# Performance work log

Hardware: AMD Instinct MI355X
Metric: run time of the kernel (lower is better)

The kernel has to match this reference:

```python
import jax, jax.numpy as jnp
import numpy as np

B, T, H, C = 64, 2048, 128, 7


def _lstm_layer(xs, W_ih, W_hh, b):
    # xs: [T, B, H_in]; PyTorch gate order i, f, g, o
    Bsz = xs.shape[1]
    Hs = W_hh.shape[1]

    def step(carry, x_t):
        h, c = carry
        gates = x_t @ W_ih.T + h @ W_hh.T + b  # [B, 4H]
        i, f, g, o = jnp.split(gates, 4, axis=-1)
        c = jax.nn.sigmoid(f) * c + jax.nn.sigmoid(i) * jnp.tanh(g)
        h = jax.nn.sigmoid(o) * jnp.tanh(c)
        return (h, c), h

    init = (jnp.zeros((Bsz, Hs), xs.dtype), jnp.zeros((Bsz, Hs), xs.dtype))
    _, ys = jax.lax.scan(step, init, xs)
    return ys  # [T, B, H]


def setup_inputs() -> dict:
    key = jax.random.key(0)
    ks = jax.random.split(key, 12)
    s = 1.0 / np.sqrt(H)
    u = lambda k, shape: jax.random.uniform(k, shape, jnp.float32, -s, s)
    x = jax.random.normal(ks[0], (B, T, 1), jnp.float32)
    lengths = jax.random.randint(ks[1], (B,), 1, T + 1, jnp.int32)
    return {
        "x": x,
        "lengths": lengths,
        "ff_w": u(ks[2], (H, 1)),
        "ff_b": u(ks[3], (H,)),
        "W_ih0": u(ks[4], (4 * H, H)),
        "W_hh0": u(ks[5], (4 * H, H)),
        "b0": u(ks[6], (4 * H,)),  # b_ih + b_hh fused
        "W_ih1": u(ks[7], (4 * H, H)),
        "W_hh1": u(ks[8], (4 * H, H)),
        "b1": u(ks[9], (4 * H,)),
        "lin_w": u(ks[10], (C, 3 * H)),
        "lin_b": u(ks[11], (C,)),
    }


def reference(x, lengths, ff_w, ff_b, W_ih0, W_hh0, b0, W_ih1, W_hh1, b1, lin_w, lin_b):
    # input projection (Linear(1, H))
    xf = x @ ff_w.T + ff_b  # [B, T, H]
    xs = jnp.transpose(xf, (1, 0, 2))  # [T, B, H]
    h1 = _lstm_layer(xs, W_ih0, W_hh0, b0)
    h2 = _lstm_layer(h1, W_ih1, W_hh1, b1)
    out = jnp.transpose(h2, (1, 0, 2))  # [B, T, H]

    # masked mean / max / last pooling over valid timesteps
    mask = jnp.arange(T)[None, :] < lengths[:, None]  # [B, T]
    mf = mask[:, :, None].astype(out.dtype)
    mean = (out * mf).sum(axis=1) / lengths[:, None].astype(out.dtype)
    mx = jnp.max(jnp.where(mask[:, :, None], out, -jnp.inf), axis=1)
    idx = jnp.broadcast_to((lengths - 1)[:, None, None], (out.shape[0], 1, out.shape[2]))
    last = jnp.take_along_axis(out, idx, axis=1)[:, 0]
    h = jnp.concatenate([mean, mx, last], axis=-1)  # [B, 3H]
    return h @ lin_w.T + lin_b  # [B, C]
```

## Files before the change

### kernel.cpp

```cpp
#include <hip/hip_runtime.h>
#include <hip/hip_fp16.h>

#define TT 2048
#define BB 64
#define HH 128
#define GG 512
#define CH 64
#define NCH (TT / CH)

typedef _Float16 f16x8 __attribute__((ext_vector_type(8)));
typedef _Float16 f16x4 __attribute__((ext_vector_type(4)));
typedef float f32x4 __attribute__((ext_vector_type(4)));

__device__ __forceinline__ float sigm(float x) {
    return __builtin_amdgcn_rcpf(1.0f + __expf(-x));
}
__device__ __forceinline__ float tanh_f(float x) {
    return 1.0f - 2.0f * __builtin_amdgcn_rcpf(1.0f + __expf(2.0f * x));
}
__device__ __forceinline__ void bar_lds() {
    asm volatile("s_waitcnt lgkmcnt(0)\n\ts_barrier" ::: "memory");
}

__device__ __forceinline__ f16x8 load_frag(const float* rowp, int kt, int lh) {
    const float4* p4 = (const float4*)(rowp + kt * 32 + lh * 8);
    float4 a = p4[0], b = p4[1];
    f16x8 f;
    f[0] = (_Float16)a.x; f[1] = (_Float16)a.y; f[2] = (_Float16)a.z; f[3] = (_Float16)a.w;
    f[4] = (_Float16)b.x; f[5] = (_Float16)b.y; f[6] = (_Float16)b.z; f[7] = (_Float16)b.w;
    return f;
}

__global__ __launch_bounds__(512, 1) void k_pipe(
    const float* __restrict__ x, const int* __restrict__ lengths,
    const float* __restrict__ ff_w, const float* __restrict__ ff_b,
    const float* __restrict__ W_ih0, const float* __restrict__ W_hh0,
    const float* __restrict__ b0, const float* __restrict__ W_ih1,
    const float* __restrict__ W_hh1, const float* __restrict__ b1,
    _Float16* __restrict__ h0g, int* __restrict__ flags,
    float* __restrict__ pooled) {
    const int tid = threadIdx.x;
    const int w = tid >> 6;
    const int lane = tid & 63;
    const int c = lane & 15;
    const int lh = lane >> 4;
    const int un = 16 * w + c;
    const bool ard = (c == 0);
    const bool wr16 = (lane < 16);

    __shared__ float xs[TT];
    __shared__ _Float16 Hb0[2][HH];
    __shared__ _Float16 Hb1[2][HH];
    __shared__ _Float16 Qs[CH][GG];

    if (blockIdx.x < BB) {
        const int b = blockIdx.x;
        for (int i = tid; i < TT; i += 512) xs[i] = x[b * TT + i];
        if (tid < 2 * HH) ((_Float16*)Hb0)[tid] = (_Float16)0.f;

        f16x8 Bf[4][4];
        float v[4], u0[4];
#pragma unroll
        for (int t2 = 0; t2 < 4; ++t2) {
            const int r = t2 * HH + un;
#pragma unroll
            for (int kt = 0; kt < 4; ++kt) Bf[t2][kt] = load_frag(W_hh0 + r * HH, kt, lh);
            const float4* wi4 = (const float4*)(W_ih0 + r * HH);
            const float4* fw4 = (const float4*)ff_w;
            const float4* fb4 = (const float4*)ff_b;
            float vv = 0.f, uu = 0.f;
#pragma unroll
            for (int m = 0; m < HH / 4; ++m) {
                float4 a = wi4[m], fw = fw4[m], fb = fb4[m];
                vv += a.x * fw.x + a.y * fw.y + a.z * fw.z + a.w * fw.w;
                uu += a.x * fb.x + a.y * fb.y + a.z * fb.z + a.w * fb.w;
            }
            v[t2] = vv;
            u0[t2] = uu + b0[r];
        }
#pragma unroll
        for (int t2 = 0; t2 < 4; ++t2)
#pragma unroll
            for (int kt = 0; kt < 4; ++kt) asm volatile("" : "+v"(Bf[t2][kt]));

        float cst0 = 0.f;
        f16x8 av[4];
#pragma unroll
        for (int kt = 0; kt < 4; ++kt) av[kt] = (f16x8){0, 0, 0, 0, 0, 0, 0, 0};
        __syncthreads();

#define PSTEP(T_, RB_)                                                          \
    do {                                                                        \
        if (ard) {                                                              \
            _Pragma("unroll") for (int kt = 0; kt < 4; ++kt)                    \
                av[kt] = *(const f16x8*)&Hb0[RB_][kt * 32 + lh * 8];            \
        }                                                                       \
        const float xt = xs[T_];                                                \
        float p[4];                                                             \
        _Pragma("unroll") for (int t2 = 0; t2 < 4; ++t2) {                      \
            f32x4 a;                                                            \
            a[0] = wr16 ? (xt * v[t2] + u0[t2]) : 0.f;                          \
            a[1] = 0.f; a[2] = 0.f; a[3] = 0.f;                                 \
            _Pragma("unroll") for (int kt = 0; kt < 4; ++kt)                    \
                a = __builtin_amdgcn_mfma_f32_16x16x32_f16(av[kt], Bf[t2][kt],  \
                                                           a, 0, 0, 0);         \
            p[t2] = a[0];                                                       \
        }                                                                       \
        float gi = sigm(p[0]), gf = sigm(p[1]);                                 \
        float gg = tanh_f(p[2]), go = sigm(p[3]);                               \
        cst0 = gf * cst0 + gi * gg;                                             \
        float h0n = go * tanh_f(cst0);                                          \
        if (wr16) {                                                             \
            Hb0[(RB_) ^ 1][un] = (_Float16)h0n;                                 \
            __builtin_nontemporal_store(                                        \
                (_Float16)h0n, h0g + ((size_t)b * TT + (T_)) * HH + un);        \
        }                                                                       \
        bar_lds();                                                              \
    } while (0)

        for (int ch = 0; ch < NCH; ++ch) {
            const int t0 = ch * CH;
            for (int j = 0; j < CH; j += 2) {
                PSTEP(t0 + j, 0);
                PSTEP(t0 + j + 1, 1);
            }
            __syncthreads();
            if (tid == 0)
                __hip_atomic_store(&flags[b * NCH + ch], ch + 1, __ATOMIC_RELEASE,
                                   __HIP_MEMORY_SCOPE_AGENT);
        }
#undef PSTEP
    } else {
        const int b = blockIdx.x - BB;
        if (tid < 2 * HH) ((_Float16*)Hb1)[tid] = (_Float16)0.f;

        f16x8 Bh[4][4];
        float bb1[4];
#pragma unroll
        for (int t2 = 0; t2 < 4; ++t2) {
#pragma unroll
            for (int kt = 0; kt < 4; ++kt)
                Bh[t2][kt] = load_frag(W_hh1 + (t2 * HH + un) * HH, kt, lh);
            bb1[t2] = b1[t2 * HH + un];
        }
#pragma unroll
        for (int t2 = 0; t2 < 4; ++t2)
#pragma unroll
            for (int kt = 0; kt < 4; ++kt) asm volatile("" : "+v"(Bh[t2][kt]));

        const int len = lengths[b];
        float cst1 = 0.f, mean = 0.f, mx = -1e30f, last = 0.f;
        f16x8 av[4];
#pragma unroll
        for (int kt = 0; kt < 4; ++kt) av[kt] = (f16x8){0, 0, 0, 0, 0, 0, 0, 0};
        __syncthreads();

#define CSTEP(T_, RB_)                                                          \
    do {                                                                        \
        const int jj = (T_) & (CH - 1);                                         \
        f16x4 qv = *(const f16x4*)&Qs[jj][un * 4];    \
        if (ard) {                                                              \
            _Pragma("unroll") for (int kt = 0; kt < 4; ++kt)                    \
                av[kt] = *(const f16x8*)&Hb1[RB_][kt * 32 + lh * 8];            \
        }                                                                       \
        float p[4];                                                             \
        _Pragma("unroll") for (int t2 = 0; t2 < 4; ++t2) {                      \
            f32x4 a;                                                            \
            a[0] = wr16 ? (float)qv[t2] : 0.f;                                  \
            a[1] = 0.f; a[2] = 0.f; a[3] = 0.f;                                 \
            _Pragma("unroll") for (int kt = 0; kt < 4; ++kt)                    \
                a = __builtin_amdgcn_mfma_f32_16x16x32_f16(av[kt], Bh[t2][kt],  \
                                                           a, 0, 0, 0);         \
            p[t2] = a[0];                                                       \
        }                                                                       \
        float gi = sigm(p[0]), gf = sigm(p[1]);                                 \
        float gg = tanh_f(p[2]), go = sigm(p[3]);                               \
        cst1 = gf * cst1 + gi * gg;                                             \
        float h1n = go * tanh_f(cst1);                                          \
        if (wr16) Hb1[(RB_) ^ 1][un] = (_Float16)h1n;                           \
        if ((T_) < len) {                                                       \
            mean += h1n;                                                        \
            mx = fmaxf(mx, h1n);                                                \
        }                                                                       \
        if ((T_) == len - 1) last = h1n;                                        \
        bar_lds();                                                              \
    } while (0)

        for (int ch = 0; ch < NCH; ++ch) {
            if (tid == 0) {
                int guard = 0;
                while (__hip_atomic_load(&flags[b * NCH + ch], __ATOMIC_ACQUIRE,
                                         __HIP_MEMORY_SCOPE_AGENT) != ch + 1) {
                    __builtin_amdgcn_s_sleep(8);
                    if (++guard > (1 << 22)) break;
                }
            }
            __syncthreads();
            f16x8 Bi[4][4];
#pragma unroll
            for (int t2 = 0; t2 < 4; ++t2)
#pragma unroll
                for (int kt = 0; kt < 4; ++kt)
                    Bi[t2][kt] = load_frag(W_ih1 + (t2 * HH + un) * HH, kt, lh);
            const _Float16* hbase = h0g + ((size_t)b * TT + ch * CH) * HH;
#pragma unroll
            for (int mt = 0; mt < 4; ++mt) {
                f16x8 am[4];
#pragma unroll
                for (int kt = 0; kt < 4; ++kt)
                    am[kt] = *(const f16x8*)(hbase + (mt * 16 + c) * HH + kt * 32 + lh * 8);
                f32x4 qa[4];
#pragma unroll
                for (int t2 = 0; t2 < 4; ++t2) {
                    qa[t2] = (f32x4){0.f, 0.f, 0.f, 0.f};
#pragma unroll
                    for (int kt = 0; kt < 4; ++kt)
                        qa[t2] = __builtin_amdgcn_mfma_f32_16x16x32_f16(
                            am[kt], Bi[t2][kt], qa[t2], 0, 0, 0);
                }
#pragma unroll
                for (int r = 0; r < 4; ++r) {
                    f16x4 qv;
#pragma unroll
                    for (int t2 = 0; t2 < 4; ++t2) qv[t2] = (_Float16)(qa[t2][r] + bb1[t2]);
                    *(f16x4*)&Qs[mt * 16 + 4 * lh + r][un * 4] = qv;
                }
            }
            __syncthreads();
            const int t0 = ch * CH;
            for (int j = 0; j < CH; j += 2) {
                CSTEP(t0 + j, 0);
                CSTEP(t0 + j + 1, 1);
            }
        }
#undef CSTEP
        if (wr16) {
            pooled[b * 384 + un] = mean / (float)len;
            pooled[b * 384 + 128 + un] = mx;
            pooled[b * 384 + 256 + un] = last;
        }
    }
}

__global__ __launch_bounds__(448) void k_head(
    const float* __restrict__ pooled, const float* __restrict__ lin_w,
    const float* __restrict__ lin_b, float* __restrict__ out) {
    int tid = threadIdx.x;
    int b = tid / 7, cc = tid % 7;
    const float* p = pooled + b * 384;
    const float* wr = lin_w + cc * 384;
    float a0 = 0.f, a1 = 0.f, a2 = 0.f, a3 = 0.f;
#pragma unroll
    for (int k = 0; k < 384; k += 4) {
        a0 += p[k + 0] * wr[k + 0];
        a1 += p[k + 1] * wr[k + 1];
        a2 += p[k + 2] * wr[k + 2];
        a3 += p[k + 3] * wr[k + 3];
    }
    out[tid] = lin_b[cc] + ((a0 + a1) + (a2 + a3));
}

extern "C" void kernel_launch(void* const* d_in, const int* in_sizes, int n_in,
                              void* d_out, int out_size, void* d_ws, size_t ws_size,
                              hipStream_t stream) {
    const float* x     = (const float*)d_in[0];
    const int*   lens  = (const int*)d_in[1];
    const float* ff_w  = (const float*)d_in[2];
    const float* ff_b  = (const float*)d_in[3];
    const float* W_ih0 = (const float*)d_in[4];
    const float* W_hh0 = (const float*)d_in[5];
    const float* b0    = (const float*)d_in[6];
    const float* W_ih1 = (const float*)d_in[7];
    const float* W_hh1 = (const float*)d_in[8];
    const float* b1    = (const float*)d_in[9];
    const float* lin_w = (const float*)d_in[10];
    const float* lin_b = (const float*)d_in[11];
    float* out = (float*)d_out;

    char* ws = (char*)d_ws;
    const size_t HBYTES = (size_t)BB * TT * HH * 2;
    _Float16* h0g = (_Float16*)ws;
    int* flags    = (int*)(ws + HBYTES);
    float* pooled = (float*)(ws + HBYTES + 8192);

    k_pipe<<<dim3(2 * BB), dim3(512), 0, stream>>>(
        x, lens, ff_w, ff_b, W_ih0, W_hh0, b0, W_ih1, W_hh1, b1, h0g, flags, pooled);
    k_head<<<dim3(1), dim3(448), 0, stream>>>(pooled, lin_w, lin_b, out);
}
```

Baseline: 1.384 ms.

## Process two batch elements per workgroup to interleave independent recurrences

Each workgroup now carries two independent batch sequences through the LSTM recurrence, halving the grid from 128 to 64 blocks. The two chains' MFMA and activation work are interleaved inside each timestep. This is meant to hide the latency of the serial per-step MFMA chain and share one barrier per step across two sequences. In exchange, each step carries twice the work, LDS use grows, and fewer CUs are occupied.

```diff
diff --git a/kernel.cpp b/kernel.cpp
--- a/kernel.cpp
+++ b/kernel.cpp
@@ -7,6 +7,7 @@
 #define GG 512
 #define CH 64
 #define NCH (TT / CH)
+#define NPB 32
 
 typedef _Float16 f16x8 __attribute__((ext_vector_type(8)));
 typedef _Float16 f16x4 __attribute__((ext_vector_type(4)));
@@ -48,15 +49,17 @@
     const bool ard = (c == 0);
     const bool wr16 = (lane < 16);
 
-    __shared__ float xs[TT];
-    __shared__ _Float16 Hb0[2][HH];
-    __shared__ _Float16 Hb1[2][HH];
-    __shared__ _Float16 Qs[CH][GG];
-
-    if (blockIdx.x < BB) {
-        const int b = blockIdx.x;
-        for (int i = tid; i < TT; i += 512) xs[i] = x[b * TT + i];
-        if (tid < 2 * HH) ((_Float16*)Hb0)[tid] = (_Float16)0.f;
+    __shared__ float xs[2][TT];
+    __shared__ _Float16 Hb0[2][2][HH];
+    __shared__ _Float16 Hb1[2][2][HH];
+    __shared__ _Float16 Qs[2][CH][GG];
+
+    if (blockIdx.x < NPB) {
+        const int p = blockIdx.x;
+        const int bA = p, bB = p + NPB;
+        for (int i = tid; i < 2 * TT; i += 512)
+            xs[i >> 11][i & (TT - 1)] = x[(i < TT ? bA : bB) * TT + (i & (TT - 1))];
+        if (tid < 4 * HH) ((_Float16*)Hb0)[tid] = (_Float16)0.f;
 
         f16x8 Bf[4][4];
         float v[4], u0[4];
@@ -83,37 +86,60 @@
 #pragma unroll
             for (int kt = 0; kt < 4; ++kt) asm volatile("" : "+v"(Bf[t2][kt]));
 
-        float cst0 = 0.f;
-        f16x8 av[4];
-#pragma unroll
-        for (int kt = 0; kt < 4; ++kt) av[kt] = (f16x8){0, 0, 0, 0, 0, 0, 0, 0};
+        float cstA = 0.f, cstB = 0.f;
+        f16x8 avA[4], avB[4];
+#pragma unroll
+        for (int kt = 0; kt < 4; ++kt) {
+            avA[kt] = (f16x8){0, 0, 0, 0, 0, 0, 0, 0};
+            avB[kt] = (f16x8){0, 0, 0, 0, 0, 0, 0, 0};
+        }
         __syncthreads();
 
 #define PSTEP(T_, RB_)                                                          \
     do {                                                                        \
         if (ard) {                                                              \
-            _Pragma("unroll") for (int kt = 0; kt < 4; ++kt)                    \
-                av[kt] = *(const f16x8*)&Hb0[RB_][kt * 32 + lh * 8];            \
-        }                                                                       \
-        const float xt = xs[T_];                                                \
-        float p[4];                                                             \
+            _Pragma("unroll") for (int kt = 0; kt < 4; ++kt) {                  \
+                avA[kt] = *(const f16x8*)&Hb0[0][RB_][kt * 32 + lh * 8];        \
+                avB[kt] = *(const f16x8*)&Hb0[1][RB_][kt * 32 + lh * 8];        \
+            }                                                                   \
+        }                                                                       \
+        const float xtA = xs[0][T_], xtB = xs[1][T_];                           \
+        float pA[4], pB[4];                                                     \
         _Pragma("unroll") for (int t2 = 0; t2 < 4; ++t2) {                      \
-            f32x4 a;                                                            \
-            a[0] = wr16 ? (xt * v[t2] + u0[t2]) : 0.f;                          \
-            a[1] = 0.f; a[2] = 0.f; a[3] = 0.f;                                 \
-            _Pragma("unroll") for (int kt = 0; kt < 4; ++kt)                    \
-                a = __builtin_amdgcn_mfma_f32_16x16x32_f16(av[kt], Bf[t2][kt],  \
-                                                           a, 0, 0, 0);         \
-            p[t2] = a[0];                                                       \
-        }                                                                       \
-        float gi = sigm(p[0]), gf = sigm(p[1]);                                 \
-        float gg = tanh_f(p[2]), go = sigm(p[3]);                               \
-        cst0 = gf * cst0 + gi * gg;                                             \
-        float h0n = go * tanh_f(cst0);                                          \
-        if (wr16) {                                                             \
-            Hb0[(RB_) ^ 1][un] = (_Float16)h0n;                                 \
-            __builtin_nontemporal_store(                                        \
-                (_Float16)h0n, h0g + ((size_t)b * TT + (T_)) * HH + un);        \
+            f32x4 aA, aB;                                                       \
+            aA[0] = wr16 ? (xtA * v[t2] + u0[t2]) : 0.f;                        \
+            aA[1] = 0.f; aA[2] = 0.f; aA[3] = 0.f;                              \
+            aB[0] = wr16 ? (xtB * v[t2] + u0[t2]) : 0.f;                        \
+            aB[1] = 0.f; aB[2] = 0.f; aB[3] = 0.f;                              \
+            _Pragma("unroll") for (int kt = 0; kt < 4; ++kt) {                  \
+                aA = __builtin_amdgcn_mfma_f32_16x16x32_f16(avA[kt],            \
+                         Bf[t2][kt], aA, 0, 0, 0);                              \
+                aB = __builtin_amdgcn_mfma_f32_16x16x32_f16(avB[kt],            \
+                         Bf[t2][kt], aB, 0, 0, 0);                              \
+            }                                                                   \
+            pA[t2] = aA[0]; pB[t2] = aB[0];                                     \
+        }                                                                       \
+        {                                                                       \
+            float gi = sigm(pA[0]), gf = sigm(pA[1]);                           \
+            float gg = tanh_f(pA[2]), go = sigm(pA[3]);                         \
+            cstA = gf * cstA + gi * gg;                                         \
+            float hn = go * tanh_f(cstA);                                       \
+            if (wr16) {                                                         \
+                Hb0[0][(RB_) ^ 1][un] = (_Float16)hn;                           \
+                __builtin_nontemporal_store(                                    \
+                    (_Float16)hn, h0g + ((size_t)bA * TT + (T_)) * HH + un);    \
+            }                                                                   \
+        }                                                                       \
+        {                                                                       \
+            float gi = sigm(pB[0]), gf = sigm(pB[1]);                           \
+            float gg = tanh_f(pB[2]), go = sigm(pB[3]);                         \
+            cstB = gf * cstB + gi * gg;                                         \
+            float hn = go * tanh_f(cstB);                                       \
+            if (wr16) {                                                         \
+                Hb0[1][(RB_) ^ 1][un] = (_Float16)hn;                           \
+                __builtin_nontemporal_store(                                    \
+                    (_Float16)hn, h0g + ((size_t)bB * TT + (T_)) * HH + un);    \
+            }                                                                   \
         }                                                                       \
         bar_lds();                                                              \
     } while (0)
@@ -126,13 +152,14 @@
             }
             __syncthreads();
             if (tid == 0)
-                __hip_atomic_store(&flags[b * NCH + ch], ch + 1, __ATOMIC_RELEASE,
+                __hip_atomic_store(&flags[p * NCH + ch], ch + 1, __ATOMIC_RELEASE,
                                    __HIP_MEMORY_SCOPE_AGENT);
         }
 #undef PSTEP
     } else {
-        const int b = blockIdx.x - BB;
-        if (tid < 2 * HH) ((_Float16*)Hb1)[tid] = (_Float16)0.f;
+        const int p = blockIdx.x - NPB;
+        const int bA = p, bB = p + NPB;
+        if (tid < 4 * HH) ((_Float16*)Hb1)[tid] = (_Float16)0.f;
 
         f16x8 Bh[4][4];
         float bb1[4];
@@ -148,48 +175,69 @@
 #pragma unroll
             for (int kt = 0; kt < 4; ++kt) asm volatile("" : "+v"(Bh[t2][kt]));
 
-        const int len = lengths[b];
-        float cst1 = 0.f, mean = 0.f, mx = -1e30f, last = 0.f;
-        f16x8 av[4];
-#pragma unroll
-        for (int kt = 0; kt < 4; ++kt) av[kt] = (f16x8){0, 0, 0, 0, 0, 0, 0, 0};
+        const int lenA = lengths[bA], lenB = lengths[bB];
+        float cstA = 0.f, cstB = 0.f;
+        float meanA = 0.f, meanB = 0.f, mxA = -1e30f, mxB = -1e30f;
+        float lastA = 0.f, lastB = 0.f;
+        f16x8 avA[4], avB[4];
+#pragma unroll
+        for (int kt = 0; kt < 4; ++kt) {
+            avA[kt] = (f16x8){0, 0, 0, 0, 0, 0, 0, 0};
+            avB[kt] = (f16x8){0, 0, 0, 0, 0, 0, 0, 0};
+        }
         __syncthreads();
 
 #define CSTEP(T_, RB_)                                                          \
     do {                                                                        \
         const int jj = (T_) & (CH - 1);                                         \
-        f16x4 qv = *(const f16x4*)&Qs[jj][un * 4];    \
+        f16x4 qA = *(const f16x4*)&Qs[0][jj][un * 4];                           \
+        f16x4 qB = *(const f16x4*)&Qs[1][jj][un * 4];                           \
         if (ard) {                                                              \
-            _Pragma("unroll") for (int kt = 0; kt < 4; ++kt)                    \
-                av[kt] = *(const f16x8*)&Hb1[RB_][kt * 32 + lh * 8];            \
-        }                                                                       \
-        float p[4];                                                             \
+            _Pragma("unroll") for (int kt = 0; kt < 4; ++kt) {                  \
+                avA[kt] = *(const f16x8*)&Hb1[0][RB_][kt * 32 + lh * 8];        \
+                avB[kt] = *(const f16x8*)&Hb1[1][RB_][kt * 32 + lh * 8];        \
+            }                                                                   \
+        }                                                                       \
+        float pA[4], pB[4];                                                     \
         _Pragma("unroll") for (int t2 = 0; t2 < 4; ++t2) {                      \
-            f32x4 a;                                                            \
-            a[0] = wr16 ? (float)qv[t2] : 0.f;                                  \
-            a[1] = 0.f; a[2] = 0.f; a[3] = 0.f;                                 \
-            _Pragma("unroll") for (int kt = 0; kt < 4; ++kt)                    \
-                a = __builtin_amdgcn_mfma_f32_16x16x32_f16(av[kt], Bh[t2][kt],  \
-                                                           a, 0, 0, 0);         \
-            p[t2] = a[0];                                                       \
-        }                                                                       \
-        float gi = sigm(p[0]), gf = sigm(p[1]);                                 \
-        float gg = tanh_f(p[2]), go = sigm(p[3]);                               \
-        cst1 = gf * cst1 + gi * gg;                                             \
-        float h1n = go * tanh_f(cst1);                                          \
-        if (wr16) Hb1[(RB_) ^ 1][un] = (_Float16)h1n;                           \
-        if ((T_) < len) {                                                       \
-            mean += h1n;                                                        \
-            mx = fmaxf(mx, h1n);                                                \
-        }                                                                       \
-        if ((T_) == len - 1) last = h1n;                                        \
+            f32x4 aA, aB;                                                       \
+            aA[0] = wr16 ? (float)qA[t2] : 0.f;                                 \
+            aA[1] = 0.f; aA[2] = 0.f; aA[3] = 0.f;                              \
+            aB[0] = wr16 ? (float)qB[t2] : 0.f;                                 \
+            aB[1] = 0.f; aB[2] = 0.f; aB[3] = 0.f;                              \
+            _Pragma("unroll") for (int kt = 0; kt < 4; ++kt) {                  \
+                aA = __builtin_amdgcn_mfma_f32_16x16x32_f16(avA[kt],            \
+                         Bh[t2][kt], aA, 0, 0, 0);                              \
+                aB = __builtin_amdgcn_mfma_f32_16x16x32_f16(avB[kt],            \
+                         Bh[t2][kt], aB, 0, 0, 0);                              \
+            }                                                                   \
+            pA[t2] = aA[0]; pB[t2] = aB[0];                                     \
+        }                                                                       \
+        {                                                                       \
+            float gi = sigm(pA[0]), gf = sigm(pA[1]);                           \
+            float gg = tanh_f(pA[2]), go = sigm(pA[3]);                         \
+            cstA = gf * cstA + gi * gg;                                         \
+            float hn = go * tanh_f(cstA);                                       \
+            if (wr16) Hb1[0][(RB_) ^ 1][un] = (_Float16)hn;                     \
+            if ((T_) < lenA) { meanA += hn; mxA = fmaxf(mxA, hn); }             \
+            if ((T_) == lenA - 1) lastA = hn;                                   \
+        }                                                                       \
+        {                                                                       \
+            float gi = sigm(pB[0]), gf = sigm(pB[1]);                           \
+            float gg = tanh_f(pB[2]), go = sigm(pB[3]);                         \
+            cstB = gf * cstB + gi * gg;                                         \
+            float hn = go * tanh_f(cstB);                                       \
+            if (wr16) Hb1[1][(RB_) ^ 1][un] = (_Float16)hn;                     \
+            if ((T_) < lenB) { meanB += hn; mxB = fmaxf(mxB, hn); }             \
+            if ((T_) == lenB - 1) lastB = hn;                                   \
+        }                                                                       \
         bar_lds();                                                              \
     } while (0)
 
         for (int ch = 0; ch < NCH; ++ch) {
             if (tid == 0) {
                 int guard = 0;
-                while (__hip_atomic_load(&flags[b * NCH + ch], __ATOMIC_ACQUIRE,
+                while (__hip_atomic_load(&flags[p * NCH + ch], __ATOMIC_ACQUIRE,
                                          __HIP_MEMORY_SCOPE_AGENT) != ch + 1) {
                     __builtin_amdgcn_s_sleep(8);
                     if (++guard > (1 << 22)) break;
@@ -202,28 +250,33 @@
 #pragma unroll
                 for (int kt = 0; kt < 4; ++kt)
                     Bi[t2][kt] = load_frag(W_ih1 + (t2 * HH + un) * HH, kt, lh);
-            const _Float16* hbase = h0g + ((size_t)b * TT + ch * CH) * HH;
-#pragma unroll
-            for (int mt = 0; mt < 4; ++mt) {
-                f16x8 am[4];
-#pragma unroll
-                for (int kt = 0; kt < 4; ++kt)
-                    am[kt] = *(const f16x8*)(hbase + (mt * 16 + c) * HH + kt * 32 + lh * 8);
-                f32x4 qa[4];
-#pragma unroll
-                for (int t2 = 0; t2 < 4; ++t2) {
-                    qa[t2] = (f32x4){0.f, 0.f, 0.f, 0.f};
+#pragma unroll
+            for (int q = 0; q < 2; ++q) {
+                const _Float16* hbase =
+                    h0g + ((size_t)(q ? bB : bA) * TT + ch * CH) * HH;
+#pragma unroll
+                for (int mt = 0; mt < 4; ++mt) {
+                    f16x8 am[4];
 #pragma unroll
                     for (int kt = 0; kt < 4; ++kt)
-                        qa[t2] = __builtin_amdgcn_mfma_f32_16x16x32_f16(
-                            am[kt], Bi[t2][kt], qa[t2], 0, 0, 0);
-                }
-#pragma unroll
-                for (int r = 0; r < 4; ++r) {
-                    f16x4 qv;
-#pragma unroll
-                    for (int t2 = 0; t2 < 4; ++t2) qv[t2] = (_Float16)(qa[t2][r] + bb1[t2]);
-                    *(f16x4*)&Qs[mt * 16 + 4 * lh + r][un * 4] = qv;
+                        am[kt] = *(const f16x8*)(hbase + (mt * 16 + c) * HH + kt * 32 + lh * 8);
+                    f32x4 qa[4];
+#pragma unroll
+                    for (int t2 = 0; t2 < 4; ++t2) {
+                        qa[t2] = (f32x4){0.f, 0.f, 0.f, 0.f};
+#pragma unroll
+                        for (int kt = 0; kt < 4; ++kt)
+                            qa[t2] = __builtin_amdgcn_mfma_f32_16x16x32_f16(
+                                am[kt], Bi[t2][kt], qa[t2], 0, 0, 0);
+                    }
+#pragma unroll
+                    for (int r = 0; r < 4; ++r) {
+                        f16x4 qv;
+#pragma unroll
+                        for (int t2 = 0; t2 < 4; ++t2)
+                            qv[t2] = (_Float16)(qa[t2][r] + bb1[t2]);
+                        *(f16x4*)&Qs[q][mt * 16 + 4 * lh + r][un * 4] = qv;
+                    }
                 }
             }
             __syncthreads();
@@ -235,9 +288,12 @@
         }
 #undef CSTEP
         if (wr16) {
-            pooled[b * 384 + un] = mean / (float)len;
-            pooled[b * 384 + 128 + un] = mx;
-            pooled[b * 384 + 256 + un] = last;
+            pooled[bA * 384 + un] = meanA / (float)lenA;
+            pooled[bA * 384 + 128 + un] = mxA;
+            pooled[bA * 384 + 256 + un] = lastA;
+            pooled[bB * 384 + un] = meanB / (float)lenB;
+            pooled[bB * 384 + 128 + un] = mxB;
+            pooled[bB * 384 + 256 + un] = lastB;
         }
     }
 }
@@ -283,7 +339,7 @@
     int* flags    = (int*)(ws + HBYTES);
     float* pooled = (float*)(ws + HBYTES + 8192);
 
-    k_pipe<<<dim3(2 * BB), dim3(512), 0, stream>>>(
+    k_pipe<<<dim3(2 * NPB), dim3(512), 0, stream>>>(
         x, lens, ff_w, ff_b, W_ih0, W_hh0, b0, W_ih1, W_hh1, b1, h0g, flags, pooled);
     k_head<<<dim3(1), dim3(448), 0, stream>>>(pooled, lin_w, lin_b, out);
 }
```

New measurement: 2.294 ms. +65.7%, slower.

## Pack two batch rows per 1024-thread block, halving grid size

Applied to the files above, without the earlier changes.

Each block now holds two independent batch sequences, one per group of 8 waves, with per-group LDS buffers. The grid shrinks from 128 to 64 blocks. The layer-1 input projection is restructured to loop over gates one at a time, which lowers register pressure under the tighter launch bounds. The block-wide barriers now couple two sequences, so each recurrence step waits for the slower of the pair and sync cost per step may rise.

```diff
diff --git a/kernel.cpp b/kernel.cpp
--- a/kernel.cpp
+++ b/kernel.cpp
@@ -7,6 +7,7 @@
 #define GG 512
 #define CH 64
 #define NCH (TT / CH)
+#define NPB 32
 
 typedef _Float16 f16x8 __attribute__((ext_vector_type(8)));
 typedef _Float16 f16x4 __attribute__((ext_vector_type(4)));
@@ -31,7 +32,7 @@
     return f;
 }
 
-__global__ __launch_bounds__(512, 1) void k_pipe(
+__global__ __launch_bounds__(1024, 4) void k_pipe(
     const float* __restrict__ x, const int* __restrict__ lengths,
     const float* __restrict__ ff_w, const float* __restrict__ ff_b,
     const float* __restrict__ W_ih0, const float* __restrict__ W_hh0,
@@ -41,22 +42,26 @@
     float* __restrict__ pooled) {
     const int tid = threadIdx.x;
     const int w = tid >> 6;
+    const int g = w >> 3;
+    const int wu = w & 7;
     const int lane = tid & 63;
     const int c = lane & 15;
     const int lh = lane >> 4;
-    const int un = 16 * w + c;
+    const int un = 16 * wu + c;
     const bool ard = (c == 0);
     const bool wr16 = (lane < 16);
 
-    __shared__ float xs[TT];
-    __shared__ _Float16 Hb0[2][HH];
-    __shared__ _Float16 Hb1[2][HH];
-    __shared__ _Float16 Qs[CH][GG];
-
-    if (blockIdx.x < BB) {
-        const int b = blockIdx.x;
-        for (int i = tid; i < TT; i += 512) xs[i] = x[b * TT + i];
-        if (tid < 2 * HH) ((_Float16*)Hb0)[tid] = (_Float16)0.f;
+    __shared__ float xs[2][TT];
+    __shared__ _Float16 Hb0[2][2][HH];
+    __shared__ _Float16 Hb1[2][2][HH];
+    __shared__ _Float16 Qs[2][CH][GG];
+
+    if (blockIdx.x < NPB) {
+        const int p = blockIdx.x;
+        const int myb = g ? (p + NPB) : p;
+        for (int i = tid; i < 2 * TT; i += 1024)
+            xs[i >> 11][i & (TT - 1)] = x[((i >> 11) ? (p + NPB) : p) * TT + (i & (TT - 1))];
+        if (tid < 4 * HH) ((_Float16*)Hb0)[tid] = (_Float16)0.f;
 
         f16x8 Bf[4][4];
         float v[4], u0[4];
@@ -93,10 +98,10 @@
     do {                                                                        \
         if (ard) {                                                              \
             _Pragma("unroll") for (int kt = 0; kt < 4; ++kt)                    \
-                av[kt] = *(const f16x8*)&Hb0[RB_][kt * 32 + lh * 8];            \
-        }                                                                       \
-        const float xt = xs[T_];                                                \
-        float p[4];                                                             \
+                av[kt] = *(const f16x8*)&Hb0[g][RB_][kt * 32 + lh * 8];         \
+        }                                                                       \
+        const float xt = xs[g][T_];                                             \
+        float p4_[4];                                                           \
         _Pragma("unroll") for (int t2 = 0; t2 < 4; ++t2) {                      \
             f32x4 a;                                                            \
             a[0] = wr16 ? (xt * v[t2] + u0[t2]) : 0.f;                          \
@@ -104,16 +109,16 @@
             _Pragma("unroll") for (int kt = 0; kt < 4; ++kt)                    \
                 a = __builtin_amdgcn_mfma_f32_16x16x32_f16(av[kt], Bf[t2][kt],  \
                                                            a, 0, 0, 0);         \
-            p[t2] = a[0];                                                       \
-        }                                                                       \
-        float gi = sigm(p[0]), gf = sigm(p[1]);                                 \
-        float gg = tanh_f(p[2]), go = sigm(p[3]);                               \
+            p4_[t2] = a[0];                                                     \
+        }                                                                       \
+        float gi = sigm(p4_[0]), gf = sigm(p4_[1]);                             \
+        float gg = tanh_f(p4_[2]), go = sigm(p4_[3]);                           \
         cst0 = gf * cst0 + gi * gg;                                             \
-        float h0n = go * tanh_f(cst0);                                          \
+        float hn = go * tanh_f(cst0);                                           \
         if (wr16) {                                                             \
-            Hb0[(RB_) ^ 1][un] = (_Float16)h0n;                                 \
+            Hb0[g][(RB_) ^ 1][un] = (_Float16)hn;                               \
             __builtin_nontemporal_store(                                        \
-                (_Float16)h0n, h0g + ((size_t)b * TT + (T_)) * HH + un);        \
+                (_Float16)hn, h0g + ((size_t)myb * TT + (T_)) * HH + un);       \
         }                                                                       \
         bar_lds();                                                              \
     } while (0)
@@ -126,13 +131,14 @@
             }
             __syncthreads();
             if (tid == 0)
-                __hip_atomic_store(&flags[b * NCH + ch], ch + 1, __ATOMIC_RELEASE,
+                __hip_atomic_store(&flags[p * NCH + ch], ch + 1, __ATOMIC_RELEASE,
                                    __HIP_MEMORY_SCOPE_AGENT);
         }
 #undef PSTEP
     } else {
-        const int b = blockIdx.x - BB;
-        if (tid < 2 * HH) ((_Float16*)Hb1)[tid] = (_Float16)0.f;
+        const int p = blockIdx.x - NPB;
+        const int myb = g ? (p + NPB) : p;
+        if (tid < 4 * HH) ((_Float16*)Hb1)[tid] = (_Float16)0.f;
 
         f16x8 Bh[4][4];
         float bb1[4];
@@ -148,8 +154,8 @@
 #pragma unroll
             for (int kt = 0; kt < 4; ++kt) asm volatile("" : "+v"(Bh[t2][kt]));
 
-        const int len = lengths[b];
-        float cst1 = 0.f, mean = 0.f, mx = -1e30f, last = 0.f;
+        const int len = lengths[myb];
+        float cst1 = 0.f, mean = 0.f, mx = -1e30f, lastv = 0.f;
         f16x8 av[4];
 #pragma unroll
         for (int kt = 0; kt < 4; ++kt) av[kt] = (f16x8){0, 0, 0, 0, 0, 0, 0, 0};
@@ -158,12 +164,12 @@
 #define CSTEP(T_, RB_)                                                          \
     do {                                                                        \
         const int jj = (T_) & (CH - 1);                                         \
-        f16x4 qv = *(const f16x4*)&Qs[jj][un * 4];    \
+        f16x4 qv = *(const f16x4*)&Qs[g][jj][un * 4];                           \
         if (ard) {                                                              \
             _Pragma("unroll") for (int kt = 0; kt < 4; ++kt)                    \
-                av[kt] = *(const f16x8*)&Hb1[RB_][kt * 32 + lh * 8];            \
-        }                                                                       \
-        float p[4];                                                             \
+                av[kt] = *(const f16x8*)&Hb1[g][RB_][kt * 32 + lh * 8];         \
+        }                                                                       \
+        float p4_[4];                                                           \
         _Pragma("unroll") for (int t2 = 0; t2 < 4; ++t2) {                      \
             f32x4 a;                                                            \
             a[0] = wr16 ? (float)qv[t2] : 0.f;                                  \
@@ -171,59 +177,49 @@
             _Pragma("unroll") for (int kt = 0; kt < 4; ++kt)                    \
                 a = __builtin_amdgcn_mfma_f32_16x16x32_f16(av[kt], Bh[t2][kt],  \
                                                            a, 0, 0, 0);         \
-            p[t2] = a[0];                                                       \
-        }                                                                       \
-        float gi = sigm(p[0]), gf = sigm(p[1]);                                 \
-        float gg = tanh_f(p[2]), go = sigm(p[3]);                               \
+            p4_[t2] = a[0];                                                     \
+        }                                                                       \
+        float gi = sigm(p4_[0]), gf = sigm(p4_[1]);                             \
+        float gg = tanh_f(p4_[2]), go = sigm(p4_[3]);                           \
         cst1 = gf * cst1 + gi * gg;                                             \
-        float h1n = go * tanh_f(cst1);                                          \
-        if (wr16) Hb1[(RB_) ^ 1][un] = (_Float16)h1n;                           \
-        if ((T_) < len) {                                                       \
-            mean += h1n;                                                        \
-            mx = fmaxf(mx, h1n);                                                \
-        }                                                                       \
-        if ((T_) == len - 1) last = h1n;                                        \
+        float hn = go * tanh_f(cst1);                                           \
+        if (wr16) Hb1[g][(RB_) ^ 1][un] = (_Float16)hn;                         \
+        if ((T_) < len) { mean += hn; mx = fmaxf(mx, hn); }                     \
+        if ((T_) == len - 1) lastv = hn;                                        \
         bar_lds();                                                              \
     } while (0)
 
         for (int ch = 0; ch < NCH; ++ch) {
             if (tid == 0) {
                 int guard = 0;
-                while (__hip_atomic_load(&flags[b * NCH + ch], __ATOMIC_ACQUIRE,
+                while (__hip_atomic_load(&flags[p * NCH + ch], __ATOMIC_ACQUIRE,
                                          __HIP_MEMORY_SCOPE_AGENT) != ch + 1) {
                     __builtin_amdgcn_s_sleep(8);
                     if (++guard > (1 << 22)) break;
                 }
             }
             __syncthreads();
-            f16x8 Bi[4][4];
-#pragma unroll
-            for (int t2 = 0; t2 < 4; ++t2)
+            const _Float16* hbase = h0g + ((size_t)myb * TT + ch * CH) * HH;
+#pragma unroll 1
+            for (int t2 = 0; t2 < 4; ++t2) {
+                f16x8 Bi[4];
 #pragma unroll
                 for (int kt = 0; kt < 4; ++kt)
-                    Bi[t2][kt] = load_frag(W_ih1 + (t2 * HH + un) * HH, kt, lh);
-            const _Float16* hbase = h0g + ((size_t)b * TT + ch * CH) * HH;
-#pragma unroll
-            for (int mt = 0; mt < 4; ++mt) {
-                f16x8 am[4];
-#pragma unroll
-                for (int kt = 0; kt < 4; ++kt)
-                    am[kt] = *(const f16x8*)(hbase + (mt * 16 + c) * HH + kt * 32 + lh * 8);
-                f32x4 qa[4];
-#pragma unroll
-                for (int t2 = 0; t2 < 4; ++t2) {
-                    qa[t2] = (f32x4){0.f, 0.f, 0.f, 0.f};
+                    Bi[kt] = load_frag(W_ih1 + (t2 * HH + un) * HH, kt, lh);
+#pragma unroll
+                for (int mt = 0; mt < 4; ++mt) {
+                    f16x8 am[4];
 #pragma unroll
                     for (int kt = 0; kt < 4; ++kt)
-                        qa[t2] = __builtin_amdgcn_mfma_f32_16x16x32_f16(
-                            am[kt], Bi[t2][kt], qa[t2], 0, 0, 0);
-                }
-#pragma unroll
-                for (int r = 0; r < 4; ++r) {
-                    f16x4 qv;
-#pragma unroll
-                    for (int t2 = 0; t2 < 4; ++t2) qv[t2] = (_Float16)(qa[t2][r] + bb1[t2]);
-                    *(f16x4*)&Qs[mt * 16 + 4 * lh + r][un * 4] = qv;
+                        am[kt] = *(const f16x8*)(hbase + (mt * 16 + c) * HH + kt * 32 + lh * 8);
+                    f32x4 qa = (f32x4){0.f, 0.f, 0.f, 0.f};
+#pragma unroll
+                    for (int kt = 0; kt < 4; ++kt)
+                        qa = __builtin_amdgcn_mfma_f32_16x16x32_f16(am[kt], Bi[kt], qa, 0, 0, 0);
+#pragma unroll
+                    for (int r = 0; r < 4; ++r)
+                        Qs[g][mt * 16 + 4 * lh + r][un * 4 + t2] =
+                            (_Float16)(qa[r] + bb1[t2]);
                 }
             }
             __syncthreads();
@@ -235,9 +231,9 @@
         }
 #undef CSTEP
         if (wr16) {
-            pooled[b * 384 + un] = mean / (float)len;
-            pooled[b * 384 + 128 + un] = mx;
-            pooled[b * 384 + 256 + un] = last;
+            pooled[myb * 384 + un] = mean / (float)len;
+            pooled[myb * 384 + 128 + un] = mx;
+            pooled[myb * 384 + 256 + un] = lastv;
         }
     }
 }
@@ -283,7 +279,7 @@
     int* flags    = (int*)(ws + HBYTES);
     float* pooled = (float*)(ws + HBYTES + 8192);
 
-    k_pipe<<<dim3(2 * BB), dim3(512), 0, stream>>>(
+    k_pipe<<<dim3(2 * NPB), dim3(1024), 0, stream>>>(
         x, lens, ff_w, ff_b, W_ih0, W_hh0, b0, W_ih1, W_hh1, b1, h0g, flags, pooled);
     k_head<<<dim3(1), dim3(448), 0, stream>>>(pooled, lin_w, lin_b, out);
 }
```

Result: slower. 3.551 ms (+156.6%).
